# Performance work log

Hardware: AMD Instinct MI355X
Metric: run time of the kernel (lower is better)

## Reference

```python
import jax, jax.numpy as jnp
import numpy as np

HEADS = 8
DIM_HEAD = 64
NUM_MEM_KV = 4

def rmsnorm(x, g):
    # F.normalize(x, dim=1) * g * sqrt(C): L2-normalize over channel dim with eps clamp
    n = jnp.sqrt(jnp.sum(x * x, axis=1, keepdims=True))
    return x / jnp.maximum(n, 1e-12) * g * (x.shape[1] ** 0.5)

def setup_inputs() -> dict:
    key = jax.random.key(0)
    ks = jax.random.split(key, 7)
    b, c, h, w = 32, 512, 32, 32
    hidden = HEADS * DIM_HEAD
    x = jax.random.normal(ks[0], (b, c, h, w), jnp.float32)
    g_in = 1.0 + 0.02 * jax.random.normal(ks[1], (1, c, 1, 1), jnp.float32)
    w_qkv = jax.random.normal(ks[2], (3 * hidden, c), jnp.float32) * (c ** -0.5)
    mem_kv = jax.random.normal(ks[3], (2, HEADS, DIM_HEAD, NUM_MEM_KV), jnp.float32)
    w_out = jax.random.normal(ks[4], (c, hidden), jnp.float32) * (hidden ** -0.5)
    b_out = 0.01 * jax.random.normal(ks[5], (c,), jnp.float32)
    g_out = 1.0 + 0.02 * jax.random.normal(ks[6], (1, c, 1, 1), jnp.float32)
    return {"x": x, "g_in": g_in, "w_qkv": w_qkv, "mem_kv": mem_kv,
            "w_out": w_out, "b_out": b_out, "g_out": g_out}

def reference(x, g_in, w_qkv, mem_kv, w_out, b_out, g_out):
    b, c, h, w = x.shape
    scale = DIM_HEAD ** -0.5
    xn = rmsnorm(x, g_in)
    # 1x1 conv (no bias) == channel GEMM
    qkv = jnp.einsum('bchw,oc->bohw', xn, w_qkv)
    q, k, v = jnp.split(qkv, 3, axis=1)
    to_heads = lambda t: t.reshape(b, HEADS, DIM_HEAD, h * w)  # b (h c) x y -> b h c (xy)
    q, k, v = map(to_heads, (q, k, v))
    mk = jnp.broadcast_to(mem_kv[0], (b,) + mem_kv[0].shape)
    mv = jnp.broadcast_to(mem_kv[1], (b,) + mem_kv[1].shape)
    k = jnp.concatenate([mk, k], axis=-1)
    v = jnp.concatenate([mv, v], axis=-1)
    q = jax.nn.softmax(q, axis=-2) * scale   # softmax over feature dim d
    k = jax.nn.softmax(k, axis=-1)           # softmax over sequence dim n
    context = jnp.einsum('bhdn,bhen->bhde', k, v)
    out = jnp.einsum('bhde,bhdn->bhen', context, q)
    out = out.reshape(b, HEADS * DIM_HEAD, h, w)
    out = jnp.einsum('bchw,oc->bohw', out, w_out) + b_out[None, :, None, None]
    return rmsnorm(out, g_out)
```

## Files before the change

### kernel.cpp

```cpp
#include <hip/hip_runtime.h>
#include <hip/hip_bf16.h>


#define AS1 __attribute__((address_space(1)))
#define AS3 __attribute__((address_space(3)))

using short8 = __attribute__((ext_vector_type(8))) short;
using usht4  = __attribute__((ext_vector_type(4))) unsigned short;
using f32x2  = __attribute__((ext_vector_type(2))) float;
using f32x4  = __attribute__((ext_vector_type(4))) float;

__device__ __forceinline__ unsigned short f2bf(float f) {
  unsigned int u = __float_as_uint(f);
  u += 0x7fffu + ((u >> 16) & 1u);
  return (unsigned short)(u >> 16);
}
__device__ __forceinline__ float bf2f(unsigned short s) {
  return __uint_as_float(((unsigned int)s) << 16);
}

__global__ __launch_bounds__(256, 2)
void xnorm_t(const float* __restrict__ X, unsigned short* __restrict__ XT) {
  __shared__ float tile[512][34];
  __shared__ float part[32][33];
  __shared__ float rloc[32];
  const int t = threadIdx.x;
  const int b = blockIdx.x >> 5;
  const int pos0 = (blockIdx.x & 31) * 32;
  const int pr = t & 7, cr = t >> 3;
  const float* xp = X + ((size_t)b * 512 + cr) * 1024 + pos0 + pr * 4;
  f32x4 ssq = {0.f, 0.f, 0.f, 0.f};
#pragma unroll
  for (int i = 0; i < 16; ++i) {
    f32x4 v = *(const f32x4*)(xp + (size_t)(i * 32) * 1024);
    ssq += v * v;
    f32x2 lo = {v.x, v.y}, hi = {v.z, v.w};
    *(f32x2*)(&tile[i * 32 + cr][pr * 4]) = lo;
    *(f32x2*)(&tile[i * 32 + cr][pr * 4 + 2]) = hi;
  }
  part[cr][pr * 4 + 0] = ssq.x;
  part[cr][pr * 4 + 1] = ssq.y;
  part[cr][pr * 4 + 2] = ssq.z;
  part[cr][pr * 4 + 3] = ssq.w;
  __syncthreads();
  if (t < 32) {
    float tot = 0.f;
#pragma unroll
    for (int j = 0; j < 32; ++j) tot += part[j][t];
    rloc[t] = 22.627416998f / fmaxf(sqrtf(tot), 1e-12f);
  }
  __syncthreads();
#pragma unroll
  for (int k = 0; k < 8; ++k) {
    const int idx = k * 256 + t;
    const int p = idx >> 6, c8 = idx & 63;
    const float r = rloc[p];
    short8 v;
#pragma unroll
    for (int j = 0; j < 8; ++j) v[j] = (short)f2bf(tile[c8 * 8 + j][p] * r);
    *(short8*)(XT + ((size_t)b * 1024 + pos0 + p) * 512 + c8 * 8) = v;
  }
}

__global__ __launch_bounds__(256, 2)
void norm_scale(const unsigned short* __restrict__ P, const float* __restrict__ G,
                float* __restrict__ O) {
  __shared__ unsigned short tile[512][68];
  __shared__ float part[2048];
  const int t = threadIdx.x;
  const int b = blockIdx.x >> 4;
  const int pos0 = (blockIdx.x & 15) * 64;
  const int pg = t & 7, cr = t >> 3;
  const unsigned short* pp = P + ((size_t)b * 512 + cr) * 1024 + pos0 + pg * 8;
  float s[8] = {};
#pragma unroll
  for (int i = 0; i < 16; ++i) {
    short8 v = *(const short8*)(pp + (size_t)(i * 32) * 1024);
    usht4 lo = {(unsigned short)v[0], (unsigned short)v[1],
                (unsigned short)v[2], (unsigned short)v[3]};
    usht4 hi = {(unsigned short)v[4], (unsigned short)v[5],
                (unsigned short)v[6], (unsigned short)v[7]};
    *(usht4*)(&tile[i * 32 + cr][pg * 8]) = lo;
    *(usht4*)(&tile[i * 32 + cr][pg * 8 + 4]) = hi;
#pragma unroll
    for (int j = 0; j < 8; ++j) {
      const float f = bf2f((unsigned short)v[j]);
      s[j] += f * f;
    }
  }
#pragma unroll
  for (int j = 0; j < 8; ++j) part[cr * 64 + pg * 8 + j] = s[j];
  __syncthreads();
  if (t < 64) {
    float tot = 0.f;
#pragma unroll
    for (int j = 0; j < 32; ++j) tot += part[j * 64 + t];
    part[t] = 22.627416998f / fmaxf(sqrtf(tot), 1e-12f);
  }
  __syncthreads();
#pragma unroll
  for (int k = 0; k < 32; ++k) {
    const int idx = k * 256 + t;
    const int c = idx >> 4, p4 = idx & 15;
    usht4 v = *(const usht4*)(&tile[c][p4 * 4]);
    const float g = G[c];
    f32x4 o;
    o.x = bf2f(v.x) * part[p4 * 4 + 0] * g;
    o.y = bf2f(v.y) * part[p4 * 4 + 1] * g;
    o.z = bf2f(v.z) * part[p4 * 4 + 2] * g;
    o.w = bf2f(v.w) * part[p4 * 4 + 3] * g;
    *(f32x4*)(O + ((size_t)b * 512 + c) * 1024 + pos0 + p4 * 4) = o;
  }
}

__global__ __launch_bounds__(256, 4)
void cast_wqkv(const float* __restrict__ W, const float* __restrict__ g,
               unsigned short* __restrict__ O) {
  int i = blockIdx.x * 256 + threadIdx.x;
  O[i] = f2bf(W[i] * g[i & 511]);
}
__global__ __launch_bounds__(256, 4)
void cast_w(const float* __restrict__ W, unsigned short* __restrict__ O, int n) {
  int i = blockIdx.x * 256 + threadIdx.x;
  if (i < n) O[i] = f2bf(W[i]);
}

template <int MTOT, bool SPLIT3, bool BIAS>
__global__ __launch_bounds__(256, 2)
void gemm_bt(const unsigned short* __restrict__ A,
             const unsigned short* __restrict__ Ball,
             unsigned short* __restrict__ O0, unsigned short* __restrict__ O1,
             unsigned short* __restrict__ O2, const float* __restrict__ bias) {
  __shared__ char smem[34816];
  unsigned short* lA = (unsigned short*)smem;
  unsigned short* lB = lA + 128 * 64;
  const int t = threadIdx.x;
  const int lane = t & 63, w = t >> 6;
  const int wm = w >> 1, wn = w & 1;
  const int mt = blockIdx.x >> 3, nt = blockIdx.x & 7;
  const int b = blockIdx.y;
  const unsigned short* Ag = A + (size_t)(mt * 128) * 512;
  const unsigned short* Bg = Ball + ((size_t)b * 1024 + (size_t)nt * 128) * 512;
  const int scol = ((lane & 7) ^ (lane >> 3)) * 8;
  f32x4 acc[4][4] = {};

  for (int kt = 0; kt < 8; ++kt) {
    const unsigned short* As = Ag + kt * 64 + scol;
    const unsigned short* Bs = Bg + kt * 64 + scol;
#pragma unroll
    for (int i = 0; i < 4; ++i) {
      const int r = w * 32 + i * 8 + (lane >> 3);
      __builtin_amdgcn_global_load_lds(
          (const AS1 unsigned int*)(As + (size_t)r * 512),
          (AS3 unsigned int*)(lA + (w * 32 + i * 8) * 64), 16, 0, 0);
      __builtin_amdgcn_global_load_lds(
          (const AS1 unsigned int*)(Bs + (size_t)r * 512),
          (AS3 unsigned int*)(lB + (w * 32 + i * 8) * 64), 16, 0, 0);
    }
    __syncthreads();
#pragma unroll
    for (int ks = 0; ks < 2; ++ks) {
      const int pch = ((ks * 4 + (lane >> 4)) ^ (lane & 7)) * 8;
      short8 af[4], bfv[4];
#pragma unroll
      for (int i = 0; i < 4; ++i)
        af[i] = *(const short8*)(lA + (wm * 64 + i * 16 + (lane & 15)) * 64 + pch);
#pragma unroll
      for (int j = 0; j < 4; ++j)
        bfv[j] = *(const short8*)(lB + (wn * 64 + j * 16 + (lane & 15)) * 64 + pch);
#pragma unroll
      for (int i = 0; i < 4; ++i)
#pragma unroll
        for (int j = 0; j < 4; ++j)
          acc[i][j] = __builtin_amdgcn_mfma_f32_16x16x32_bf16(af[i], bfv[j],
                                                              acc[i][j], 0, 0, 0);
    }
    __syncthreads();
  }

  unsigned short* Cst = (unsigned short*)smem;
#pragma unroll
  for (int i = 0; i < 4; ++i)
#pragma unroll
    for (int j = 0; j < 4; ++j)
#pragma unroll
      for (int r = 0; r < 4; ++r) {
        const int row = wm * 64 + i * 16 + (lane >> 4) * 4 + r;
        const int col = wn * 64 + j * 16 + (lane & 15);
        float v = acc[i][j][r];
        if (BIAS) v += bias[mt * 128 + row];
        Cst[row * 136 + col] = f2bf(v);
      }
  __syncthreads();
  unsigned short* Og;
  if (SPLIT3) {
    const int sec = mt >> 2;
    unsigned short* base = (sec == 0) ? O0 : ((sec == 1) ? O1 : O2);
    Og = base + ((size_t)b * 512 + (size_t)(mt & 3) * 128) * 1024 + (size_t)nt * 128;
  } else {
    Og = O0 + ((size_t)b * MTOT + (size_t)mt * 128) * 1024 + (size_t)nt * 128;
  }
#pragma unroll
  for (int k = 0; k < 8; ++k) {
    const int f = t + k * 256;
    const int row = f >> 4, c8 = f & 15;
    short8 v = *(const short8*)(Cst + row * 136 + c8 * 8);
    *(short8*)(Og + (size_t)row * 1024 + c8 * 8) = v;
  }
}

__global__ __launch_bounds__(256, 2)
void attn_kernel(const unsigned short* __restrict__ Qp,
                 const unsigned short* __restrict__ Kp,
                 const unsigned short* __restrict__ Vp,
                 const float* __restrict__ memkv,
                 unsigned short* __restrict__ outT) {
  __shared__ char smem[36608];
  unsigned short* bufA = (unsigned short*)smem;
  unsigned short* bufB = (unsigned short*)(smem + 9216);
  float* Pl   = (float*)(smem + 18432);
  float* Pc   = (float*)(smem + 18432);
  float* csS  = (float*)(smem + 21504);
  float* msum = (float*)(smem + 35072);
  float* rsI  = (float*)(smem + 36096);
  const int t = threadIdx.x;
  const int lane = t & 63, wave = t >> 6;
  const int b = blockIdx.x >> 3, h = blockIdx.x & 7;
  const size_t hb = ((size_t)b * 512 + (size_t)h * 64) * 1024;
  const unsigned short* Qg = Qp + hb;
  const unsigned short* Kg = Kp + hb;
  const unsigned short* Vg = Vp + hb;
  const float* mk = memkv + (size_t)h * 256;
  const float* mv = memkv + 2048 + (size_t)h * 256;

  float rsum[2] = {0.f, 0.f};
  f32x4 cacc[4] = {};

  for (int it = 0; it < 17; ++it) {
    if (it == 0) {
      const int d = t & 63, j = t >> 6;
      const float ev = __expf(mk[d * 4 + j]);
      msum[d * 4 + j] = ev;
      bufA[d * 72 + j] = f2bf(ev);
      bufB[d * 72 + j] = f2bf(mv[d * 4 + j]);
      for (int c2 = 4 + j; c2 < 64; c2 += 4) {
        bufA[d * 72 + c2] = 0;
        bufB[d * 72 + c2] = 0;
      }
    } else {
      const int c0 = (it - 1) * 64;
#pragma unroll
      for (int z = 0; z < 2; ++z) {
        const int d = z * 32 + (t >> 3), ch = t & 7;
        short8 kv = *(const short8*)(Kg + (size_t)d * 1024 + c0 + ch * 8);
        short8 pk;
        float ssum = 0.f;
#pragma unroll
        for (int j = 0; j < 8; ++j) {
          const float e = __expf(bf2f((unsigned short)kv[j]));
          ssum += e;
          pk[j] = (short)f2bf(e);
        }
        rsum[z] += ssum;
        *(short8*)(bufA + d * 72 + ch * 8) = pk;
        short8 vv = *(const short8*)(Vg + (size_t)d * 1024 + c0 + ch * 8);
        *(short8*)(bufB + d * 72 + ch * 8) = vv;
      }
    }
    __syncthreads();
#pragma unroll
    for (int ks = 0; ks < 2; ++ks) {
      short8 a = *(const short8*)(bufA + (wave * 16 + (lane & 15)) * 72 +
                                  ks * 32 + (lane >> 4) * 8);
#pragma unroll
      for (int et = 0; et < 4; ++et) {
        short8 bb = *(const short8*)(bufB + (et * 16 + (lane & 15)) * 72 +
                                     ks * 32 + (lane >> 4) * 8);
        cacc[et] = __builtin_amdgcn_mfma_f32_16x16x32_bf16(a, bb, cacc[et], 0, 0, 0);
      }
    }
    __syncthreads();
  }

  Pl[t]       = rsum[0];
  Pl[256 + t] = rsum[1];
  __syncthreads();
  if (t < 64) {
    float s = 0.f;
#pragma unroll
    for (int ch = 0; ch < 8; ++ch) s += Pl[t * 8 + ch];
    s += msum[t * 4] + msum[t * 4 + 1] + msum[t * 4 + 2] + msum[t * 4 + 3];
    rsI[t] = 1.0f / s;
  }
  __syncthreads();

  unsigned short* CT = bufB;
#pragma unroll
  for (int et = 0; et < 4; ++et)
#pragma unroll
    for (int r = 0; r < 4; ++r) {
      const int d = wave * 16 + (lane >> 4) * 4 + r;
      const int e = et * 16 + (lane & 15);
      CT[e * 72 + d] = f2bf(cacc[et][r] * rsI[d]);
    }
  __syncthreads();

  short8 a0 = *(const short8*)(CT + (wave * 16 + (lane & 15)) * 72 + (lane >> 4) * 8);
  short8 a1 = *(const short8*)(CT + (wave * 16 + (lane & 15)) * 72 + 32 + (lane >> 4) * 8);
  unsigned short* oBase = outT + (size_t)b * 1024 * 512 + h * 64;

  for (int pt = 0; pt < 16; ++pt) {
    {
      const int p = lane, dq = wave;
      float cp = 0.f;
#pragma unroll
      for (int i2 = 0; i2 < 8; ++i2) {
        const int d0 = dq * 16 + i2 * 2;
        const float e0 = __expf(bf2f(Qg[(size_t)d0 * 1024 + pt * 64 + p]));
        const float e1 = __expf(bf2f(Qg[(size_t)(d0 + 1) * 1024 + pt * 64 + p]));
        cp += e0 + e1;
        const unsigned int pk =
            (unsigned int)f2bf(e0) | ((unsigned int)f2bf(e1) << 16);
        *(unsigned int*)(bufA + p * 72 + d0) = pk;
      }
      Pc[dq * 64 + p] = cp;
    }
    __syncthreads();
    if (t < 64) csS[t] = 0.125f / (Pc[t] + Pc[64 + t] + Pc[128 + t] + Pc[192 + t]);
    __syncthreads();
#pragma unroll
    for (int ps = 0; ps < 4; ++ps) {
      f32x4 oc = {};
      short8 b0 = *(const short8*)(bufA + (ps * 16 + (lane & 15)) * 72 + (lane >> 4) * 8);
      short8 b1 = *(const short8*)(bufA + (ps * 16 + (lane & 15)) * 72 + 32 + (lane >> 4) * 8);
      oc = __builtin_amdgcn_mfma_f32_16x16x32_bf16(a0, b0, oc, 0, 0, 0);
      oc = __builtin_amdgcn_mfma_f32_16x16x32_bf16(a1, b1, oc, 0, 0, 0);
      const float cs = csS[ps * 16 + (lane & 15)];
      const unsigned long long pk =
          (unsigned long long)f2bf(oc[0] * cs) |
          ((unsigned long long)f2bf(oc[1] * cs) << 16) |
          ((unsigned long long)f2bf(oc[2] * cs) << 32) |
          ((unsigned long long)f2bf(oc[3] * cs) << 48);
      const int p = pt * 64 + ps * 16 + (lane & 15);
      *(unsigned long long*)(oBase + (size_t)p * 512 + wave * 16 + (lane >> 4) * 4) = pk;
    }
    __syncthreads();
  }
}

extern "C" void kernel_launch(void* const* d_in, const int* in_sizes, int n_in,
                              void* d_out, int out_size, void* d_ws, size_t ws_size,
                              hipStream_t stream) {
  (void)in_sizes; (void)n_in; (void)out_size; (void)ws_size;
  const float* x     = (const float*)d_in[0];
  const float* g_in  = (const float*)d_in[1];
  const float* w_qkv = (const float*)d_in[2];
  const float* memkv = (const float*)d_in[3];
  const float* w_out = (const float*)d_in[4];
  const float* b_out = (const float*)d_in[5];
  const float* g_out = (const float*)d_in[6];
  float* out = (float*)d_out;

  char* ws = (char*)d_ws;
  unsigned short* wqb = (unsigned short*)(ws + 262144);
  unsigned short* wob = (unsigned short*)(ws + 1835008);
  unsigned short* xnT = (unsigned short*)(ws + 2359296);
  unsigned short* Qp  = (unsigned short*)(ws + 35913728);
  unsigned short* outT = xnT;
  unsigned short* pre  = Qp;
  unsigned short* Kp  = (unsigned short*)d_out;
  unsigned short* Vp  = (unsigned short*)d_out + 16777216;

  xnorm_t<<<1024, 256, 0, stream>>>(x, xnT);
  cast_wqkv<<<3072, 256, 0, stream>>>(w_qkv, g_in, wqb);
  cast_w<<<1024, 256, 0, stream>>>(w_out, wob, 262144);
  gemm_bt<1536, true, false><<<dim3(96, 32), 256, 0, stream>>>(
      wqb, xnT, Qp, Kp, Vp, nullptr);
  attn_kernel<<<256, 256, 0, stream>>>(Qp, Kp, Vp, memkv, outT);
  gemm_bt<512, false, true><<<dim3(32, 32), 256, 0, stream>>>(
      wob, outT, pre, nullptr, nullptr, b_out);
  norm_scale<<<512, 256, 0, stream>>>(pre, g_out, out);
}
```

Measured before the change: 256.4 us.

## Split attention into context and output kernels for more parallelism; swizzle GEMM epilogue LDS

Result: slower. 262.7 us (+2.4%).

```diff
diff --git a/kernel.cpp b/kernel.cpp
--- a/kernel.cpp
+++ b/kernel.cpp
@@ -131,7 +131,7 @@
              const unsigned short* __restrict__ Ball,
              unsigned short* __restrict__ O0, unsigned short* __restrict__ O1,
              unsigned short* __restrict__ O2, const float* __restrict__ bias) {
-  __shared__ char smem[34816];
+  __shared__ char smem[32768];
   unsigned short* lA = (unsigned short*)smem;
   unsigned short* lB = lA + 128 * 64;
   const int t = threadIdx.x;
@@ -189,7 +189,7 @@
         const int col = wn * 64 + j * 16 + (lane & 15);
         float v = acc[i][j][r];
         if (BIAS) v += bias[mt * 128 + row];
-        Cst[row * 136 + col] = f2bf(v);
+        Cst[row * 128 + ((((col >> 3) ^ (row & 7)) << 3) | (col & 7))] = f2bf(v);
       }
   __syncthreads();
   unsigned short* Og;
@@ -204,30 +204,26 @@
   for (int k = 0; k < 8; ++k) {
     const int f = t + k * 256;
     const int row = f >> 4, c8 = f & 15;
-    short8 v = *(const short8*)(Cst + row * 136 + c8 * 8);
+    short8 v = *(const short8*)(Cst + row * 128 + ((c8 ^ (row & 7)) << 3));
     *(short8*)(Og + (size_t)row * 1024 + c8 * 8) = v;
   }
 }
 
 __global__ __launch_bounds__(256, 2)
-void attn_kernel(const unsigned short* __restrict__ Qp,
-                 const unsigned short* __restrict__ Kp,
-                 const unsigned short* __restrict__ Vp,
-                 const float* __restrict__ memkv,
-                 unsigned short* __restrict__ outT) {
+void attn_ctx(const unsigned short* __restrict__ Kp,
+              const unsigned short* __restrict__ Vp,
+              const float* __restrict__ memkv,
+              unsigned short* __restrict__ VpW) {
   __shared__ char smem[36608];
   unsigned short* bufA = (unsigned short*)smem;
   unsigned short* bufB = (unsigned short*)(smem + 9216);
   float* Pl   = (float*)(smem + 18432);
-  float* Pc   = (float*)(smem + 18432);
-  float* csS  = (float*)(smem + 21504);
   float* msum = (float*)(smem + 35072);
   float* rsI  = (float*)(smem + 36096);
   const int t = threadIdx.x;
   const int lane = t & 63, wave = t >> 6;
   const int b = blockIdx.x >> 3, h = blockIdx.x & 7;
   const size_t hb = ((size_t)b * 512 + (size_t)h * 64) * 1024;
-  const unsigned short* Qg = Qp + hb;
   const unsigned short* Kg = Kp + hb;
   const unsigned short* Vg = Vp + hb;
   const float* mk = memkv + (size_t)h * 256;
@@ -305,11 +301,46 @@
     }
   __syncthreads();
 
-  short8 a0 = *(const short8*)(CT + (wave * 16 + (lane & 15)) * 72 + (lane >> 4) * 8);
-  short8 a1 = *(const short8*)(CT + (wave * 16 + (lane & 15)) * 72 + 32 + (lane >> 4) * 8);
+  unsigned short* ctxG = VpW + hb;
+#pragma unroll
+  for (int k = 0; k < 2; ++k) {
+    const int idx = k * 256 + t;
+    const int e = idx >> 3, ch = idx & 7;
+    short8 v = *(const short8*)(CT + e * 72 + ch * 8);
+    *(short8*)(ctxG + e * 64 + ch * 8) = v;
+  }
+}
+
+__global__ __launch_bounds__(256, 4)
+void attn_out(const unsigned short* __restrict__ Qp,
+              const unsigned short* __restrict__ ctxP,
+              unsigned short* __restrict__ outT) {
+  __shared__ unsigned short ctx[64 * 72];
+  __shared__ unsigned short eq[64 * 72];
+  __shared__ float Pc[256];
+  __shared__ float csS[64];
+  const int t = threadIdx.x;
+  const int lane = t & 63, wave = t >> 6;
+  const int b = blockIdx.x >> 5, h = (blockIdx.x >> 2) & 7, ptc = blockIdx.x & 3;
+  const size_t hb = ((size_t)b * 512 + (size_t)h * 64) * 1024;
+  const unsigned short* Qg = Qp + hb;
+  const unsigned short* ctxG = ctxP + hb;
+
+#pragma unroll
+  for (int k = 0; k < 2; ++k) {
+    const int idx = k * 256 + t;
+    const int e = idx >> 3, ch = idx & 7;
+    short8 v = *(const short8*)(ctxG + e * 64 + ch * 8);
+    *(short8*)(ctx + e * 72 + ch * 8) = v;
+  }
+  __syncthreads();
+
+  short8 a0 = *(const short8*)(ctx + (wave * 16 + (lane & 15)) * 72 + (lane >> 4) * 8);
+  short8 a1 = *(const short8*)(ctx + (wave * 16 + (lane & 15)) * 72 + 32 + (lane >> 4) * 8);
   unsigned short* oBase = outT + (size_t)b * 1024 * 512 + h * 64;
 
-  for (int pt = 0; pt < 16; ++pt) {
+  for (int it = 0; it < 4; ++it) {
+    const int pt = ptc * 4 + it;
     {
       const int p = lane, dq = wave;
       float cp = 0.f;
@@ -321,7 +352,7 @@
         cp += e0 + e1;
         const unsigned int pk =
             (unsigned int)f2bf(e0) | ((unsigned int)f2bf(e1) << 16);
-        *(unsigned int*)(bufA + p * 72 + d0) = pk;
+        *(unsigned int*)(eq + p * 72 + d0) = pk;
       }
       Pc[dq * 64 + p] = cp;
     }
@@ -331,8 +362,8 @@
 #pragma unroll
     for (int ps = 0; ps < 4; ++ps) {
       f32x4 oc = {};
-      short8 b0 = *(const short8*)(bufA + (ps * 16 + (lane & 15)) * 72 + (lane >> 4) * 8);
-      short8 b1 = *(const short8*)(bufA + (ps * 16 + (lane & 15)) * 72 + 32 + (lane >> 4) * 8);
+      short8 b0 = *(const short8*)(eq + (ps * 16 + (lane & 15)) * 72 + (lane >> 4) * 8);
+      short8 b1 = *(const short8*)(eq + (ps * 16 + (lane & 15)) * 72 + 32 + (lane >> 4) * 8);
       oc = __builtin_amdgcn_mfma_f32_16x16x32_bf16(a0, b0, oc, 0, 0, 0);
       oc = __builtin_amdgcn_mfma_f32_16x16x32_bf16(a1, b1, oc, 0, 0, 0);
       const float cs = csS[ps * 16 + (lane & 15)];
@@ -362,8 +393,8 @@
   float* out = (float*)d_out;
 
   char* ws = (char*)d_ws;
-  unsigned short* wqb = (unsigned short*)(ws + 262144);
-  unsigned short* wob = (unsigned short*)(ws + 1835008);
+  unsigned short* wob = (unsigned short*)ws;
+  unsigned short* wqb = (unsigned short*)(ws + 524288);
   unsigned short* xnT = (unsigned short*)(ws + 2359296);
   unsigned short* Qp  = (unsigned short*)(ws + 35913728);
   unsigned short* outT = xnT;
@@ -376,7 +407,8 @@
   cast_w<<<1024, 256, 0, stream>>>(w_out, wob, 262144);
   gemm_bt<1536, true, false><<<dim3(96, 32), 256, 0, stream>>>(
       wqb, xnT, Qp, Kp, Vp, nullptr);
-  attn_kernel<<<256, 256, 0, stream>>>(Qp, Kp, Vp, memkv, outT);
+  attn_ctx<<<256, 256, 0, stream>>>(Kp, Vp, memkv, Vp);
+  attn_out<<<1024, 256, 0, stream>>>(Qp, Vp, outT);
   gemm_bt<512, false, true><<<dim3(32, 32), 256, 0, stream>>>(
       wob, outT, pre, nullptr, nullptr, b_out);
   norm_scale<<<512, 256, 0, stream>>>(pre, g_out, out);
```

## Prefetch K/V/Q registers in attention and XOR-swizzle GEMM epilogue staging

Applied to the files above, without the earlier changes.

After: 254.6 us. No clear change (-0.7%).

```diff
diff --git a/kernel.cpp b/kernel.cpp
--- a/kernel.cpp
+++ b/kernel.cpp
@@ -131,7 +131,7 @@
              const unsigned short* __restrict__ Ball,
              unsigned short* __restrict__ O0, unsigned short* __restrict__ O1,
              unsigned short* __restrict__ O2, const float* __restrict__ bias) {
-  __shared__ char smem[34816];
+  __shared__ char smem[32768];
   unsigned short* lA = (unsigned short*)smem;
   unsigned short* lB = lA + 128 * 64;
   const int t = threadIdx.x;
@@ -189,7 +189,7 @@
         const int col = wn * 64 + j * 16 + (lane & 15);
         float v = acc[i][j][r];
         if (BIAS) v += bias[mt * 128 + row];
-        Cst[row * 136 + col] = f2bf(v);
+        Cst[row * 128 + ((((col >> 3) ^ (row & 7)) << 3) | (col & 7))] = f2bf(v);
       }
   __syncthreads();
   unsigned short* Og;
@@ -204,7 +204,7 @@
   for (int k = 0; k < 8; ++k) {
     const int f = t + k * 256;
     const int row = f >> 4, c8 = f & 15;
-    short8 v = *(const short8*)(Cst + row * 136 + c8 * 8);
+    short8 v = *(const short8*)(Cst + row * 128 + ((c8 ^ (row & 7)) << 3));
     *(short8*)(Og + (size_t)row * 1024 + c8 * 8) = v;
   }
 }
@@ -236,6 +236,16 @@
   float rsum[2] = {0.f, 0.f};
   f32x4 cacc[4] = {};
 
+  const int dz = t >> 3, ch = t & 7;
+  const unsigned short* Kr0 = Kg + (size_t)dz * 1024 + ch * 8;
+  const unsigned short* Kr1 = Kg + (size_t)(32 + dz) * 1024 + ch * 8;
+  const unsigned short* Vr0 = Vg + (size_t)dz * 1024 + ch * 8;
+  const unsigned short* Vr1 = Vg + (size_t)(32 + dz) * 1024 + ch * 8;
+  short8 kr0 = *(const short8*)(Kr0);
+  short8 kr1 = *(const short8*)(Kr1);
+  short8 vr0 = *(const short8*)(Vr0);
+  short8 vr1 = *(const short8*)(Vr1);
+
   for (int it = 0; it < 17; ++it) {
     if (it == 0) {
       const int d = t & 63, j = t >> 6;
@@ -248,26 +258,41 @@
         bufB[d * 72 + c2] = 0;
       }
     } else {
-      const int c0 = (it - 1) * 64;
-#pragma unroll
-      for (int z = 0; z < 2; ++z) {
-        const int d = z * 32 + (t >> 3), ch = t & 7;
-        short8 kv = *(const short8*)(Kg + (size_t)d * 1024 + c0 + ch * 8);
-        short8 pk;
-        float ssum = 0.f;
+      short8 k0 = kr0, k1 = kr1, v0 = vr0, v1 = vr1;
+      if (it < 16) {
+        const int c0n = it * 64;
+        kr0 = *(const short8*)(Kr0 + c0n);
+        kr1 = *(const short8*)(Kr1 + c0n);
+        vr0 = *(const short8*)(Vr0 + c0n);
+        vr1 = *(const short8*)(Vr1 + c0n);
+      }
+      {
+        short8 pk; float ss = 0.f;
 #pragma unroll
         for (int j = 0; j < 8; ++j) {
-          const float e = __expf(bf2f((unsigned short)kv[j]));
-          ssum += e;
+          const float e = __expf(bf2f((unsigned short)k0[j]));
+          ss += e;
           pk[j] = (short)f2bf(e);
         }
-        rsum[z] += ssum;
-        *(short8*)(bufA + d * 72 + ch * 8) = pk;
-        short8 vv = *(const short8*)(Vg + (size_t)d * 1024 + c0 + ch * 8);
-        *(short8*)(bufB + d * 72 + ch * 8) = vv;
-      }
-    }
-    __syncthreads();
+        rsum[0] += ss;
+        *(short8*)(bufA + dz * 72 + ch * 8) = pk;
+        *(short8*)(bufB + dz * 72 + ch * 8) = v0;
+      }
+      {
+        short8 pk; float ss = 0.f;
+#pragma unroll
+        for (int j = 0; j < 8; ++j) {
+          const float e = __expf(bf2f((unsigned short)k1[j]));
+          ss += e;
+          pk[j] = (short)f2bf(e);
+        }
+        rsum[1] += ss;
+        *(short8*)(bufA + (32 + dz) * 72 + ch * 8) = pk;
+        *(short8*)(bufB + (32 + dz) * 72 + ch * 8) = v1;
+      }
+    }
+    __syncthreads();
+    __builtin_amdgcn_s_setprio(1);
 #pragma unroll
     for (int ks = 0; ks < 2; ++ks) {
       short8 a = *(const short8*)(bufA + (wave * 16 + (lane & 15)) * 72 +
@@ -279,6 +304,7 @@
         cacc[et] = __builtin_amdgcn_mfma_f32_16x16x32_bf16(a, bb, cacc[et], 0, 0, 0);
       }
     }
+    __builtin_amdgcn_s_setprio(0);
     __syncthreads();
   }
 
@@ -288,7 +314,7 @@
   if (t < 64) {
     float s = 0.f;
 #pragma unroll
-    for (int ch = 0; ch < 8; ++ch) s += Pl[t * 8 + ch];
+    for (int ch2 = 0; ch2 < 8; ++ch2) s += Pl[t * 8 + ch2];
     s += msum[t * 4] + msum[t * 4 + 1] + msum[t * 4 + 2] + msum[t * 4 + 3];
     rsI[t] = 1.0f / s;
   }
@@ -309,15 +335,32 @@
   short8 a1 = *(const short8*)(CT + (wave * 16 + (lane & 15)) * 72 + 32 + (lane >> 4) * 8);
   unsigned short* oBase = outT + (size_t)b * 1024 * 512 + h * 64;
 
+  const int p = lane, dq = wave;
+  unsigned short qv[16];
+#pragma unroll
+  for (int i2 = 0; i2 < 8; ++i2) {
+    qv[2 * i2]     = Qg[(size_t)(dq * 16 + i2 * 2) * 1024 + p];
+    qv[2 * i2 + 1] = Qg[(size_t)(dq * 16 + i2 * 2 + 1) * 1024 + p];
+  }
   for (int pt = 0; pt < 16; ++pt) {
+    unsigned short q[16];
+#pragma unroll
+    for (int j = 0; j < 16; ++j) q[j] = qv[j];
+    if (pt < 15) {
+      const int qo = (pt + 1) * 64;
+#pragma unroll
+      for (int i2 = 0; i2 < 8; ++i2) {
+        qv[2 * i2]     = Qg[(size_t)(dq * 16 + i2 * 2) * 1024 + qo + p];
+        qv[2 * i2 + 1] = Qg[(size_t)(dq * 16 + i2 * 2 + 1) * 1024 + qo + p];
+      }
+    }
     {
-      const int p = lane, dq = wave;
       float cp = 0.f;
 #pragma unroll
       for (int i2 = 0; i2 < 8; ++i2) {
         const int d0 = dq * 16 + i2 * 2;
-        const float e0 = __expf(bf2f(Qg[(size_t)d0 * 1024 + pt * 64 + p]));
-        const float e1 = __expf(bf2f(Qg[(size_t)(d0 + 1) * 1024 + pt * 64 + p]));
+        const float e0 = __expf(bf2f(q[2 * i2]));
+        const float e1 = __expf(bf2f(q[2 * i2 + 1]));
         cp += e0 + e1;
         const unsigned int pk =
             (unsigned int)f2bf(e0) | ((unsigned int)f2bf(e1) << 16);
@@ -328,6 +371,7 @@
     __syncthreads();
     if (t < 64) csS[t] = 0.125f / (Pc[t] + Pc[64 + t] + Pc[128 + t] + Pc[192 + t]);
     __syncthreads();
+    __builtin_amdgcn_s_setprio(1);
 #pragma unroll
     for (int ps = 0; ps < 4; ++ps) {
       f32x4 oc = {};
@@ -341,9 +385,10 @@
           ((unsigned long long)f2bf(oc[1] * cs) << 16) |
           ((unsigned long long)f2bf(oc[2] * cs) << 32) |
           ((unsigned long long)f2bf(oc[3] * cs) << 48);
-      const int p = pt * 64 + ps * 16 + (lane & 15);
-      *(unsigned long long*)(oBase + (size_t)p * 512 + wave * 16 + (lane >> 4) * 4) = pk;
-    }
+      const int pp2 = pt * 64 + ps * 16 + (lane & 15);
+      *(unsigned long long*)(oBase + (size_t)pp2 * 512 + wave * 16 + (lane >> 4) * 4) = pk;
+    }
+    __builtin_amdgcn_s_setprio(0);
     __syncthreads();
   }
 }
@@ -362,8 +407,8 @@
   float* out = (float*)d_out;
 
   char* ws = (char*)d_ws;
-  unsigned short* wqb = (unsigned short*)(ws + 262144);
-  unsigned short* wob = (unsigned short*)(ws + 1835008);
+  unsigned short* wob = (unsigned short*)ws;
+  unsigned short* wqb = (unsigned short*)(ws + 524288);
   unsigned short* xnT = (unsigned short*)(ws + 2359296);
   unsigned short* Qp  = (unsigned short*)(ws + 35913728);
   unsigned short* outT = xnT;
```
